# Kernel tuning notes

Hardware: AMD Instinct MI355X
Metric: run time of the kernel (lower is better)

Reference implementation:

```python
import jax, jax.numpy as jnp
import numpy as np

NUM_RELATIONS = 4


def setup_inputs() -> dict:
    key = jax.random.key(0)
    ks = jax.random.split(key, 16)
    N, E, IN, H, OUT = 50000, 1000000, 64, 64, 32
    inp = {
        "x": jax.random.normal(ks[0], (N, IN), dtype=jnp.float32),
        "edge_index": jax.random.randint(ks[1], (2, E), 0, N, dtype=jnp.int32),
        "edge_type": jax.random.randint(ks[2], (E,), 0, NUM_RELATIONS, dtype=jnp.int32),
        "edge_weight": jax.random.uniform(ks[3], (E,), dtype=jnp.float32),
        # RGCN layer 1
        "W1": jax.random.normal(ks[4], (NUM_RELATIONS, IN, H), dtype=jnp.float32) * 0.02,
        "W01": jax.random.normal(ks[5], (IN, H), dtype=jnp.float32) * 0.02,
        # GroupEnhance 1
        "alpha1": jnp.float32(0.5),
        "projW1": jax.random.normal(ks[6], (H, H), dtype=jnp.float32) * 0.02,
        "projb1": jnp.zeros((H,), dtype=jnp.float32),
        # RGCN layer 2
        "W2": jax.random.normal(ks[7], (NUM_RELATIONS, H, H), dtype=jnp.float32) * 0.02,
        "W02": jax.random.normal(ks[8], (H, H), dtype=jnp.float32) * 0.02,
        # GroupEnhance 2
        "alpha2": jnp.float32(0.5),
        "projW2": jax.random.normal(ks[9], (H, H), dtype=jnp.float32) * 0.02,
        "projb2": jnp.zeros((H,), dtype=jnp.float32),
        # output head
        "outW": jax.random.normal(ks[10], (H, OUT), dtype=jnp.float32) * 0.02,
        "outb": jnp.zeros((OUT,), dtype=jnp.float32),
    }
    return inp


def _rgcn(x, src, dst, edge_type, edge_weight, W, W0, deg, num_nodes):
    # per-relation transform: msg_e = x[src_e] @ W[edge_type_e]
    xs = x[src]  # [E, d]
    msg = jnp.zeros((xs.shape[0], W.shape[-1]), dtype=x.dtype)
    for r in range(NUM_RELATIONS):
        msg = msg + jnp.where((edge_type == r)[:, None], xs @ W[r], 0.0)
    msg = msg * edge_weight[:, None]
    agg = jax.ops.segment_sum(msg, dst, num_segments=num_nodes)
    out = x @ W0 + agg
    return out / deg[:, None]


def _group(x, src, dst, edge_weight, alpha, projW, projb, deg, num_nodes):
    msg = x[src] * edge_weight[:, None]
    agg = jax.ops.segment_sum(msg, dst, num_segments=num_nodes) / deg[:, None]
    return x + alpha * (agg @ projW + projb)


def reference(x, edge_index, edge_type, edge_weight, W1, W01, alpha1, projW1,
              projb1, W2, W02, alpha2, projW2, projb2, outW, outb):
    num_nodes = x.shape[0]
    src, dst = edge_index[0], edge_index[1]
    # degree (unweighted in-degree, clamped to 1), shared by all layers
    deg = jax.ops.segment_sum(jnp.ones_like(edge_weight), dst,
                              num_segments=num_nodes)
    deg = jnp.clip(deg, 1.0)
    h = jax.nn.relu(_rgcn(x, src, dst, edge_type, edge_weight, W1, W01, deg, num_nodes))
    h = _group(h, src, dst, edge_weight, alpha1, projW1, projb1, deg, num_nodes)
    h = jax.nn.relu(_rgcn(h, src, dst, edge_type, edge_weight, W2, W02, deg, num_nodes))
    h = _group(h, src, dst, edge_weight, alpha2, projW2, projb2, deg, num_nodes)
    return h @ outW + outb
```

## Files before the change

### kernel.cpp

```cpp
#include <hip/hip_runtime.h>


#define PART_EPB 2048

__global__ __launch_bounds__(256) void bucket_hist(const int* __restrict__ ei,
                                                   int* __restrict__ bcnt,
                                                   int E, int NB) {
    __shared__ int h[1024];
    for (int i = threadIdx.x; i < 1024; i += 256) h[i] = 0;
    __syncthreads();
    int base = blockIdx.x * PART_EPB;
#pragma unroll
    for (int k = 0; k < PART_EPB / 256; ++k) {
        int e = base + k * 256 + threadIdx.x;
        if (e < E) atomicAdd(&h[ei[E + e] >> 8], 1);
    }
    __syncthreads();
    for (int i = threadIdx.x; i < NB; i += 256)
        if (h[i]) atomicAdd(&bcnt[i], h[i]);
}

__global__ __launch_bounds__(1024) void bucket_scan(const int* __restrict__ bcnt,
                                                    int* __restrict__ bofs,
                                                    int* __restrict__ bcur,
                                                    int NB, int E) {
    __shared__ int lds[1024];
    int tid = threadIdx.x;
    int v = (tid < NB) ? bcnt[tid] : 0;
    lds[tid] = v;
    __syncthreads();
    int acc = v;
    for (int off = 1; off < 1024; off <<= 1) {
        int t = (tid >= off) ? lds[tid - off] : 0;
        __syncthreads();
        acc += t;
        lds[tid] = acc;
        __syncthreads();
    }
    int excl = acc - v;
    if (tid < NB) { bofs[tid] = excl; bcur[tid] = excl; }
    if (tid == 0) bofs[NB] = E;
}

__global__ __launch_bounds__(256) void partition(const int* __restrict__ ei,
                                                 const int* __restrict__ et,
                                                 const float* __restrict__ ew,
                                                 int* __restrict__ gcur,
                                                 int2* __restrict__ recA,
                                                 int* __restrict__ recB,
                                                 int E, int NB) {
    __shared__ int hist[1024];
    __shared__ int base[1024];
    const int tid = threadIdx.x;
    const int blockBase = blockIdx.x * PART_EPB;
    for (int i = tid; i < 1024; i += 256) hist[i] = 0;
    __syncthreads();
#pragma unroll
    for (int k = 0; k < PART_EPB / 256; ++k) {
        int e = blockBase + k * 256 + tid;
        if (e < E) atomicAdd(&hist[ei[E + e] >> 8], 1);
    }
    __syncthreads();
    for (int i = tid; i < NB; i += 256) {
        int h = hist[i];
        base[i] = h ? atomicAdd(&gcur[i], h) : 0;
    }
    __syncthreads();
    for (int i = tid; i < 1024; i += 256) hist[i] = 0;
    __syncthreads();
#pragma unroll
    for (int k = 0; k < PART_EPB / 256; ++k) {
        int e = blockBase + k * 256 + tid;
        if (e >= E) continue;
        int dst = ei[E + e];
        int b = dst >> 8;
        int pos = base[b] + atomicAdd(&hist[b], 1);
        recA[pos] = make_int2(ei[e], __float_as_int(ew[e]));
        recB[pos] = dst * 4 + et[e];
    }
}

__global__ __launch_bounds__(256) void bucket_fill(
    const int2* __restrict__ recA, const int* __restrict__ recB,
    const int* __restrict__ bofs, int* __restrict__ rp2, int2* __restrict__ pw,
    int N) {
    __shared__ int cnt[1024];
    __shared__ int cur[1024];
    __shared__ int wsum[4];
    const int b = blockIdx.x;
    const int tid = threadIdx.x;
    const int beg = bofs[b], end = bofs[b + 1];
    const int rebase = b << 10;
    for (int j = 0; j < 4; ++j) cnt[tid * 4 + j] = 0;
    __syncthreads();
    for (int i = beg + tid; i < end; i += 256)
        atomicAdd(&cnt[recB[i] - rebase], 1);
    __syncthreads();
    int v[4];
    int s = 0;
#pragma unroll
    for (int j = 0; j < 4; ++j) { v[j] = cnt[tid * 4 + j]; s += v[j]; }
    int lane = tid & 63, wid = tid >> 6;
    int ws = s;
#pragma unroll
    for (int off = 1; off < 64; off <<= 1) {
        int t = __shfl_up(ws, off);
        if (lane >= off) ws += t;
    }
    if (lane == 63) wsum[wid] = ws;
    __syncthreads();
    int wb = 0;
    for (int w = 0; w < wid; ++w) wb += wsum[w];
    int run = beg + wb + ws - s;
#pragma unroll
    for (int j = 0; j < 4; ++j) {
        int idx = rebase + tid * 4 + j;
        if (idx <= 4 * N) rp2[idx] = run;
        cur[tid * 4 + j] = run;
        run += v[j];
    }
    __syncthreads();
    for (int i = beg + tid; i < end; i += 256) {
        int l = recB[i] - rebase;
        int p = atomicAdd(&cur[l], 1);
        pw[p] = recA[i];
    }
}

__device__ __forceinline__ float4 quad_reduce(float4 a) {
#pragma unroll
    for (int off = 16; off < 64; off <<= 1) {
        a.x += __shfl_xor(a.x, off);
        a.y += __shfl_xor(a.y, off);
        a.z += __shfl_xor(a.z, off);
        a.w += __shfl_xor(a.w, off);
    }
    return a;
}

__device__ __forceinline__ void fma4(float4& a, float w, const float4& x) {
    a.x += w * x.x; a.y += w * x.y; a.z += w * x.z; a.w += w * x.w;
}

__device__ __forceinline__ unsigned short f2bf(float f) {
    unsigned u = __float_as_uint(f);
    unsigned r = u + 0x7fffu + ((u >> 16) & 1u);
    return (unsigned short)(r >> 16);
}

__device__ __forceinline__ float bf2f(unsigned short h) {
    return __uint_as_float(((unsigned)h) << 16);
}

__device__ __forceinline__ float4 bf2f4(ushort4 h) {
    return make_float4(bf2f(h.x), bf2f(h.y), bf2f(h.z), bf2f(h.w));
}

__global__ __launch_bounds__(256) void cast_bf16(const float* __restrict__ in,
                                                 unsigned short* __restrict__ out,
                                                 int n4) {
    int i = blockIdx.x * 256 + threadIdx.x;
    if (i >= n4) return;
    float4 v = reinterpret_cast<const float4*>(in)[i];
    reinterpret_cast<ushort4*>(out)[i] =
        make_ushort4(f2bf(v.x), f2bf(v.y), f2bf(v.z), f2bf(v.w));
}

template <int REL>
__global__ __launch_bounds__(256) void gather_k(
    const unsigned short* __restrict__ Xb, const int* __restrict__ rp2,
    const int2* __restrict__ pw, void* __restrict__ outp, int N) {
    int node = blockIdx.x * 4 + (threadIdx.x >> 6);
    if (node >= N) return;
    int lane = threadIdx.x & 63;
    int q = lane >> 4, m = lane & 15;
    const int4 sv = *reinterpret_cast<const int4*>(rp2 + node * 4);
    const int s0 = sv.x, s1 = sv.y, s2 = sv.z, s3 = sv.w;
    const int s4 = rp2[node * 4 + 4];
    float4 A0 = make_float4(0.f, 0.f, 0.f, 0.f);
    float4 A1 = make_float4(0.f, 0.f, 0.f, 0.f);
    float4 A2 = make_float4(0.f, 0.f, 0.f, 0.f);
    float4 A3 = make_float4(0.f, 0.f, 0.f, 0.f);

    auto accum = [&](int idx, int slot, int2 e, const float4& xv) {
        float w = __int_as_float(e.y);
        if (REL) {
            fma4(A0, (idx < s1) ? w : 0.f, xv);
            fma4(A1, (idx >= s1 && idx < s2) ? w : 0.f, xv);
            fma4(A2, (idx >= s2 && idx < s3) ? w : 0.f, xv);
            fma4(A3, (idx >= s3) ? w : 0.f, xv);
        } else {
            if (slot == 0) fma4(A0, w, xv);
            else if (slot == 1) fma4(A1, w, xv);
            else if (slot == 2) fma4(A2, w, xv);
            else fma4(A3, w, xv);
        }
    };

    int i = s0 + q;
    for (; i + 12 < s4; i += 16) {
        int2 e0 = pw[i];
        int2 e1 = pw[i + 4];
        int2 e2 = pw[i + 8];
        int2 e3 = pw[i + 12];
        ushort4 h0 = *reinterpret_cast<const ushort4*>(Xb + (size_t)e0.x * 64 + m * 4);
        ushort4 h1 = *reinterpret_cast<const ushort4*>(Xb + (size_t)e1.x * 64 + m * 4);
        ushort4 h2 = *reinterpret_cast<const ushort4*>(Xb + (size_t)e2.x * 64 + m * 4);
        ushort4 h3 = *reinterpret_cast<const ushort4*>(Xb + (size_t)e3.x * 64 + m * 4);
        accum(i, 0, e0, bf2f4(h0));
        accum(i + 4, 1, e1, bf2f4(h1));
        accum(i + 8, 2, e2, bf2f4(h2));
        accum(i + 12, 3, e3, bf2f4(h3));
    }
    for (; i + 4 < s4; i += 8) {
        int2 e0 = pw[i];
        int2 e1 = pw[i + 4];
        ushort4 h0 = *reinterpret_cast<const ushort4*>(Xb + (size_t)e0.x * 64 + m * 4);
        ushort4 h1 = *reinterpret_cast<const ushort4*>(Xb + (size_t)e1.x * 64 + m * 4);
        accum(i, 0, e0, bf2f4(h0));
        accum(i + 4, 1, e1, bf2f4(h1));
    }
    if (i < s4) {
        int2 e0 = pw[i];
        ushort4 h0 = *reinterpret_cast<const ushort4*>(Xb + (size_t)e0.x * 64 + m * 4);
        accum(i, 0, e0, bf2f4(h0));
    }

    if (REL) {
        A0 = quad_reduce(A0);
        A1 = quad_reduce(A1);
        A2 = quad_reduce(A2);
        A3 = quad_reduce(A3);
        float4 o = (q == 0) ? A0 : (q == 1) ? A1 : (q == 2) ? A2 : A3;
        ushort4 h = make_ushort4(f2bf(o.x), f2bf(o.y), f2bf(o.z), f2bf(o.w));
        *reinterpret_cast<ushort4*>((unsigned short*)outp +
                                    (size_t)node * 256 + q * 64 + m * 4) = h;
    } else {
        A0.x += A1.x + A2.x + A3.x;
        A0.y += A1.y + A2.y + A3.y;
        A0.z += A1.z + A2.z + A3.z;
        A0.w += A1.w + A2.w + A3.w;
        A0 = quad_reduce(A0);
        if (q == 0)
            *reinterpret_cast<float4*>((float*)outp + (size_t)node * 64 + m * 4) = A0;
    }
}

template <int MODE>
__global__ __launch_bounds__(256) void node_gemm(
    const float* __restrict__ X, const float* __restrict__ AGG,
    const unsigned short* __restrict__ AGGh, const float* __restrict__ B0,
    const float* __restrict__ B1, const float* __restrict__ bias,
    const float* __restrict__ bias2, const float* __restrict__ alphap,
    const int* __restrict__ rp2, float* __restrict__ OUT,
    unsigned short* __restrict__ OUTb, int N) {
    __shared__ float As[64][68];
    __shared__ float Bs[64][64];
    const int tid = threadIdx.x;
    const int tx = tid & 15, ty = tid >> 4;
    const int row0 = blockIdx.x * 64;
    float acc[4][4] = {};

    const int nchunks = (MODE == 0) ? 5 : 1;
    for (int c = 0; c < nchunks; ++c) {
        const float* B;
        if (MODE == 0) B = (c == 0) ? B0 : B1 + (size_t)(c - 1) * 64 * 64;
        else           B = B0;
        if (c) __syncthreads();
#pragma unroll
        for (int q = 0; q < 4; ++q) {
            int f = q * 256 + tid;
            int r = f >> 4;
            int c4 = (f & 15) << 2;
            int vr = row0 + r;
            float4 v = make_float4(0.f, 0.f, 0.f, 0.f);
            if (MODE == 0 && c > 0) {
                if (vr < N) {
                    ushort4 hv = *reinterpret_cast<const ushort4*>(
                        AGGh + (size_t)vr * 256 + (c - 1) * 64 + c4);
                    v = bf2f4(hv);
                }
            } else {
                const float* A = (MODE == 0) ? X : AGG;
                if (vr < N) v = *reinterpret_cast<const float4*>(A + (size_t)vr * 64 + c4);
            }
            *reinterpret_cast<float4*>(&As[r][c4]) = v;
            *reinterpret_cast<float4*>(&Bs[r][c4]) =
                *reinterpret_cast<const float4*>(B + (size_t)r * 64 + c4);
        }
        __syncthreads();
#pragma unroll 8
        for (int k = 0; k < 64; ++k) {
            float4 b = *reinterpret_cast<const float4*>(&Bs[k][tx * 4]);
            float a0 = As[ty * 4 + 0][k];
            float a1 = As[ty * 4 + 1][k];
            float a2 = As[ty * 4 + 2][k];
            float a3 = As[ty * 4 + 3][k];
            acc[0][0] += a0 * b.x; acc[0][1] += a0 * b.y; acc[0][2] += a0 * b.z; acc[0][3] += a0 * b.w;
            acc[1][0] += a1 * b.x; acc[1][1] += a1 * b.y; acc[1][2] += a1 * b.z; acc[1][3] += a1 * b.w;
            acc[2][0] += a2 * b.x; acc[2][1] += a2 * b.y; acc[2][2] += a2 * b.z; acc[2][3] += a2 * b.w;
            acc[3][0] += a3 * b.x; acc[3][1] += a3 * b.y; acc[3][2] += a3 * b.z; acc[3][3] += a3 * b.w;
        }
    }

    const float alpha = (MODE == 1 || MODE == 3) ? alphap[0] : 0.f;

    if (MODE == 3) {
        __syncthreads();
#pragma unroll
        for (int i = 0; i < 4; ++i) {
            int vr = row0 + ty * 4 + i;
            float dg = 1.f;
            if (vr < N) dg = fmaxf((float)(rp2[vr * 4 + 4] - rp2[vr * 4]), 1.f);
#pragma unroll
            for (int j = 0; j < 4; ++j) {
                int col = tx * 4 + j;
                float g = 0.f;
                if (vr < N)
                    g = X[(size_t)vr * 64 + col] + alpha * (acc[i][j] / dg + bias[col]);
                As[ty * 4 + i][col] = g;
            }
        }
#pragma unroll
        for (int t = 0; t < 2; ++t) {
            int idx = tid * 2 + t;
            int r = idx >> 3;
            int c4 = (idx & 7) << 2;
            *reinterpret_cast<float4*>(&Bs[r][c4]) =
                *reinterpret_cast<const float4*>(B1 + (size_t)r * 32 + c4);
        }
        __syncthreads();
        float acc2[4][2] = {};
#pragma unroll 8
        for (int k = 0; k < 64; ++k) {
            float b0 = Bs[k][tx * 2];
            float b1 = Bs[k][tx * 2 + 1];
#pragma unroll
            for (int i = 0; i < 4; ++i) {
                float a = As[ty * 4 + i][k];
                acc2[i][0] += a * b0;
                acc2[i][1] += a * b1;
            }
        }
#pragma unroll
        for (int i = 0; i < 4; ++i) {
            int vr = row0 + ty * 4 + i;
            if (vr >= N) continue;
#pragma unroll
            for (int j = 0; j < 2; ++j) {
                int col = tx * 2 + j;
                OUT[(size_t)vr * 32 + col] = acc2[i][j] + bias2[col];
            }
        }
        return;
    }

#pragma unroll
    for (int i = 0; i < 4; ++i) {
        int vr = row0 + ty * 4 + i;
        if (vr >= N) continue;
        float dg = fmaxf((float)(rp2[vr * 4 + 4] - rp2[vr * 4]), 1.f);
        float4 o;
#pragma unroll
        for (int j = 0; j < 4; ++j) {
            int col = tx * 4 + j;
            float v;
            if (MODE == 0) {
                v = fmaxf(acc[i][j] / dg, 0.f);
            } else {
                v = X[(size_t)vr * 64 + col] + alpha * (acc[i][j] / dg + bias[col]);
            }
            OUT[(size_t)vr * 64 + col] = v;
            (&o.x)[j] = v;
        }
        *reinterpret_cast<ushort4*>(OUTb + (size_t)vr * 64 + tx * 4) =
            make_ushort4(f2bf(o.x), f2bf(o.y), f2bf(o.z), f2bf(o.w));
    }
}

extern "C" void kernel_launch(void* const* d_in, const int* in_sizes, int n_in,
                              void* d_out, int out_size, void* d_ws, size_t ws_size,
                              hipStream_t stream) {
    const float* x      = (const float*)d_in[0];
    const int*   ei     = (const int*)d_in[1];
    const int*   et     = (const int*)d_in[2];
    const float* ew     = (const float*)d_in[3];
    const float* W1     = (const float*)d_in[4];
    const float* W01    = (const float*)d_in[5];
    const float* alpha1 = (const float*)d_in[6];
    const float* projW1 = (const float*)d_in[7];
    const float* projb1 = (const float*)d_in[8];
    const float* W2     = (const float*)d_in[9];
    const float* W02    = (const float*)d_in[10];
    const float* alpha2 = (const float*)d_in[11];
    const float* projW2 = (const float*)d_in[12];
    const float* projb2 = (const float*)d_in[13];
    const float* outW   = (const float*)d_in[14];
    const float* outb   = (const float*)d_in[15];
    const int N = in_sizes[0] / 64;
    const int E = in_sizes[2];
    const int M = 4 * N;
    const int NB = (N + 255) >> 8;

    int*   bcnt = (int*)d_ws;
    int*   bofs = bcnt + 1024;
    int*   bcur = bofs + 1032;
    int*   rp2  = bcur + 1024;
    int2*  pw   = (int2*)(rp2 + ((M + 2) & ~1));
    float* aggRegion = (float*)(pw + E);
    unsigned short* aggH = (unsigned short*)aggRegion;
    float* aggF = aggRegion + (size_t)N * 128;
    unsigned short* xb = (unsigned short*)(aggRegion + (size_t)N * 192);
    unsigned short* hb = (unsigned short*)(aggRegion + (size_t)N * 224);
    int2*  recA = (int2*)aggRegion;
    int*   recB = (int*)(recA + E);
    float* hbuf = aggRegion + (size_t)N * 256;
    float* gbuf = hbuf + (size_t)N * 64;

    const int gatherBlocks = (N + 3) / 4;
    const int gemmBlocks = (N + 63) / 64;
    const int pBlocks = (E + PART_EPB - 1) / PART_EPB;

    hipMemsetAsync(bcnt, 0, 1024 * sizeof(int), stream);
    bucket_hist<<<pBlocks, 256, 0, stream>>>(ei, bcnt, E, NB);
    bucket_scan<<<1, 1024, 0, stream>>>(bcnt, bofs, bcur, NB, E);
    partition<<<pBlocks, 256, 0, stream>>>(ei, et, ew, bcur, recA, recB, E, NB);
    bucket_fill<<<NB, 256, 0, stream>>>(recA, recB, bofs, rp2, pw, N);
    cast_bf16<<<(N * 16 + 255) / 256, 256, 0, stream>>>(x, xb, N * 16);

    gather_k<1><<<gatherBlocks, 256, 0, stream>>>(xb, rp2, pw, aggH, N);
    node_gemm<0><<<gemmBlocks, 256, 0, stream>>>(x, nullptr, aggH, W01, W1, nullptr, nullptr, nullptr, rp2, hbuf, hb, N);
    gather_k<0><<<gatherBlocks, 256, 0, stream>>>(hb, rp2, pw, aggF, N);
    node_gemm<1><<<gemmBlocks, 256, 0, stream>>>(hbuf, aggF, nullptr, projW1, nullptr, projb1, nullptr, alpha1, rp2, gbuf, xb , N);

    gather_k<1><<<gatherBlocks, 256, 0, stream>>>(xb , rp2, pw, aggH, N);
    node_gemm<0><<<gemmBlocks, 256, 0, stream>>>(gbuf, nullptr, aggH, W02, W2, nullptr, nullptr, nullptr, rp2, hbuf, hb, N);
    gather_k<0><<<gatherBlocks, 256, 0, stream>>>(hb, rp2, pw, aggF, N);
    node_gemm<3><<<gemmBlocks, 256, 0, stream>>>(hbuf, aggF, nullptr, projW2, outW, projb2, outb, alpha2, rp2, (float*)d_out, nullptr, N);
}
```

Before: 400.2 us.

## Transpose GEMM A tile, register-prefetch next chunk, read bf16 self input

Rewrites the node_gemm inner loop to keep the A tile transposed in shared memory, so each k step reads four rows with one float4 load instead of four scalar loads. In MODE 0 the next chunk's A and B tiles are prefetched into registers while the current chunk computes, which overlaps global loads with FMAs. The self-loop term now reads the bf16 copy of the node features instead of fp32, halving that read but lowering the precision of the root-weight product. The transposed stores into shared memory are scattered and may cause bank conflicts.

Result: slower. 427.0 us (+6.7%).

```diff
diff --git a/kernel.cpp b/kernel.cpp
--- a/kernel.cpp
+++ b/kernel.cpp
@@ -248,58 +248,96 @@
 
 template <int MODE>
 __global__ __launch_bounds__(256) void node_gemm(
-    const float* __restrict__ X, const float* __restrict__ AGG,
-    const unsigned short* __restrict__ AGGh, const float* __restrict__ B0,
-    const float* __restrict__ B1, const float* __restrict__ bias,
-    const float* __restrict__ bias2, const float* __restrict__ alphap,
-    const int* __restrict__ rp2, float* __restrict__ OUT,
-    unsigned short* __restrict__ OUTb, int N) {
-    __shared__ float As[64][68];
+    const float* __restrict__ Xf, const float* __restrict__ AGGf,
+    const unsigned short* __restrict__ Xb0, const unsigned short* __restrict__ AGGh,
+    const float* __restrict__ B0, const float* __restrict__ B1,
+    const float* __restrict__ bias, const float* __restrict__ bias2,
+    const float* __restrict__ alphap, const int* __restrict__ rp2,
+    float* __restrict__ OUT, unsigned short* __restrict__ OUTb, int N) {
+    __shared__ float AsT[64][68];
     __shared__ float Bs[64][64];
     const int tid = threadIdx.x;
     const int tx = tid & 15, ty = tid >> 4;
     const int row0 = blockIdx.x * 64;
     float acc[4][4] = {};
 
-    const int nchunks = (MODE == 0) ? 5 : 1;
-    for (int c = 0; c < nchunks; ++c) {
-        const float* B;
-        if (MODE == 0) B = (c == 0) ? B0 : B1 + (size_t)(c - 1) * 64 * 64;
-        else           B = B0;
-        if (c) __syncthreads();
+    if (MODE == 0) {
+        ushort4 ph[4];
+        float4 pbv[4];
 #pragma unroll
         for (int q = 0; q < 4; ++q) {
             int f = q * 256 + tid;
-            int r = f >> 4;
-            int c4 = (f & 15) << 2;
+            int r = f >> 4, c4 = (f & 15) << 2;
+            int vr = row0 + r;
+            ph[q] = make_ushort4(0, 0, 0, 0);
+            if (vr < N)
+                ph[q] = *reinterpret_cast<const ushort4*>(Xb0 + (size_t)vr * 64 + c4);
+            pbv[q] = *reinterpret_cast<const float4*>(B0 + (size_t)r * 64 + c4);
+        }
+#pragma unroll
+        for (int c = 0; c < 5; ++c) {
+            __syncthreads();
+#pragma unroll
+            for (int q = 0; q < 4; ++q) {
+                int f = q * 256 + tid;
+                int r = f >> 4, c4 = (f & 15) << 2;
+                float4 v = bf2f4(ph[q]);
+                AsT[c4 + 0][r] = v.x;
+                AsT[c4 + 1][r] = v.y;
+                AsT[c4 + 2][r] = v.z;
+                AsT[c4 + 3][r] = v.w;
+                *reinterpret_cast<float4*>(&Bs[r][c4]) = pbv[q];
+            }
+            if (c < 4) {
+                const unsigned short* An = AGGh + (size_t)c * 64;
+                const float* Bn = B1 + (size_t)c * 4096;
+#pragma unroll
+                for (int q = 0; q < 4; ++q) {
+                    int f = q * 256 + tid;
+                    int r = f >> 4, c4 = (f & 15) << 2;
+                    int vr = row0 + r;
+                    ph[q] = make_ushort4(0, 0, 0, 0);
+                    if (vr < N)
+                        ph[q] = *reinterpret_cast<const ushort4*>(
+                            An + (size_t)vr * 256 + c4);
+                    pbv[q] = *reinterpret_cast<const float4*>(Bn + (size_t)r * 64 + c4);
+                }
+            }
+            __syncthreads();
+#pragma unroll 8
+            for (int k = 0; k < 64; ++k) {
+                float4 a = *reinterpret_cast<const float4*>(&AsT[k][ty * 4]);
+                float4 b = *reinterpret_cast<const float4*>(&Bs[k][tx * 4]);
+                acc[0][0] += a.x * b.x; acc[0][1] += a.x * b.y; acc[0][2] += a.x * b.z; acc[0][3] += a.x * b.w;
+                acc[1][0] += a.y * b.x; acc[1][1] += a.y * b.y; acc[1][2] += a.y * b.z; acc[1][3] += a.y * b.w;
+                acc[2][0] += a.z * b.x; acc[2][1] += a.z * b.y; acc[2][2] += a.z * b.z; acc[2][3] += a.z * b.w;
+                acc[3][0] += a.w * b.x; acc[3][1] += a.w * b.y; acc[3][2] += a.w * b.z; acc[3][3] += a.w * b.w;
+            }
+        }
+    } else {
+#pragma unroll
+        for (int q = 0; q < 4; ++q) {
+            int f = q * 256 + tid;
+            int r = f >> 4, c4 = (f & 15) << 2;
             int vr = row0 + r;
             float4 v = make_float4(0.f, 0.f, 0.f, 0.f);
-            if (MODE == 0 && c > 0) {
-                if (vr < N) {
-                    ushort4 hv = *reinterpret_cast<const ushort4*>(
-                        AGGh + (size_t)vr * 256 + (c - 1) * 64 + c4);
-                    v = bf2f4(hv);
-                }
-            } else {
-                const float* A = (MODE == 0) ? X : AGG;
-                if (vr < N) v = *reinterpret_cast<const float4*>(A + (size_t)vr * 64 + c4);
-            }
-            *reinterpret_cast<float4*>(&As[r][c4]) = v;
+            if (vr < N) v = *reinterpret_cast<const float4*>(AGGf + (size_t)vr * 64 + c4);
+            AsT[c4 + 0][r] = v.x;
+            AsT[c4 + 1][r] = v.y;
+            AsT[c4 + 2][r] = v.z;
+            AsT[c4 + 3][r] = v.w;
             *reinterpret_cast<float4*>(&Bs[r][c4]) =
-                *reinterpret_cast<const float4*>(B + (size_t)r * 64 + c4);
+                *reinterpret_cast<const float4*>(B0 + (size_t)r * 64 + c4);
         }
         __syncthreads();
 #pragma unroll 8
         for (int k = 0; k < 64; ++k) {
+            float4 a = *reinterpret_cast<const float4*>(&AsT[k][ty * 4]);
             float4 b = *reinterpret_cast<const float4*>(&Bs[k][tx * 4]);
-            float a0 = As[ty * 4 + 0][k];
-            float a1 = As[ty * 4 + 1][k];
-            float a2 = As[ty * 4 + 2][k];
-            float a3 = As[ty * 4 + 3][k];
-            acc[0][0] += a0 * b.x; acc[0][1] += a0 * b.y; acc[0][2] += a0 * b.z; acc[0][3] += a0 * b.w;
-            acc[1][0] += a1 * b.x; acc[1][1] += a1 * b.y; acc[1][2] += a1 * b.z; acc[1][3] += a1 * b.w;
-            acc[2][0] += a2 * b.x; acc[2][1] += a2 * b.y; acc[2][2] += a2 * b.z; acc[2][3] += a2 * b.w;
-            acc[3][0] += a3 * b.x; acc[3][1] += a3 * b.y; acc[3][2] += a3 * b.z; acc[3][3] += a3 * b.w;
+            acc[0][0] += a.x * b.x; acc[0][1] += a.x * b.y; acc[0][2] += a.x * b.z; acc[0][3] += a.x * b.w;
+            acc[1][0] += a.y * b.x; acc[1][1] += a.y * b.y; acc[1][2] += a.y * b.z; acc[1][3] += a.y * b.w;
+            acc[2][0] += a.z * b.x; acc[2][1] += a.z * b.y; acc[2][2] += a.z * b.z; acc[2][3] += a.z * b.w;
+            acc[3][0] += a.w * b.x; acc[3][1] += a.w * b.y; acc[3][2] += a.w * b.z; acc[3][3] += a.w * b.w;
         }
     }
 
@@ -317,8 +355,8 @@
                 int col = tx * 4 + j;
                 float g = 0.f;
                 if (vr < N)
-                    g = X[(size_t)vr * 64 + col] + alpha * (acc[i][j] / dg + bias[col]);
-                As[ty * 4 + i][col] = g;
+                    g = Xf[(size_t)vr * 64 + col] + alpha * (acc[i][j] / dg + bias[col]);
+                AsT[col][ty * 4 + i] = g;
             }
         }
 #pragma unroll
@@ -333,14 +371,13 @@
         float acc2[4][2] = {};
 #pragma unroll 8
         for (int k = 0; k < 64; ++k) {
+            float4 a = *reinterpret_cast<const float4*>(&AsT[k][ty * 4]);
             float b0 = Bs[k][tx * 2];
             float b1 = Bs[k][tx * 2 + 1];
-#pragma unroll
-            for (int i = 0; i < 4; ++i) {
-                float a = As[ty * 4 + i][k];
-                acc2[i][0] += a * b0;
-                acc2[i][1] += a * b1;
-            }
+            acc2[0][0] += a.x * b0; acc2[0][1] += a.x * b1;
+            acc2[1][0] += a.y * b0; acc2[1][1] += a.y * b1;
+            acc2[2][0] += a.z * b0; acc2[2][1] += a.z * b1;
+            acc2[3][0] += a.w * b0; acc2[3][1] += a.w * b1;
         }
 #pragma unroll
         for (int i = 0; i < 4; ++i) {
@@ -368,7 +405,7 @@
             if (MODE == 0) {
                 v = fmaxf(acc[i][j] / dg, 0.f);
             } else {
-                v = X[(size_t)vr * 64 + col] + alpha * (acc[i][j] / dg + bias[col]);
+                v = Xf[(size_t)vr * 64 + col] + alpha * (acc[i][j] / dg + bias[col]);
             }
             OUT[(size_t)vr * 64 + col] = v;
             (&o.x)[j] = v;
@@ -429,12 +466,12 @@
     cast_bf16<<<(N * 16 + 255) / 256, 256, 0, stream>>>(x, xb, N * 16);
 
     gather_k<1><<<gatherBlocks, 256, 0, stream>>>(xb, rp2, pw, aggH, N);
-    node_gemm<0><<<gemmBlocks, 256, 0, stream>>>(x, nullptr, aggH, W01, W1, nullptr, nullptr, nullptr, rp2, hbuf, hb, N);
+    node_gemm<0><<<gemmBlocks, 256, 0, stream>>>(nullptr, nullptr, xb, aggH, W01, W1, nullptr, nullptr, nullptr, rp2, hbuf, hb, N);
     gather_k<0><<<gatherBlocks, 256, 0, stream>>>(hb, rp2, pw, aggF, N);
-    node_gemm<1><<<gemmBlocks, 256, 0, stream>>>(hbuf, aggF, nullptr, projW1, nullptr, projb1, nullptr, alpha1, rp2, gbuf, xb , N);
+    node_gemm<1><<<gemmBlocks, 256, 0, stream>>>(hbuf, aggF, nullptr, nullptr, projW1, nullptr, projb1, nullptr, alpha1, rp2, gbuf, xb , N);
 
     gather_k<1><<<gatherBlocks, 256, 0, stream>>>(xb , rp2, pw, aggH, N);
-    node_gemm<0><<<gemmBlocks, 256, 0, stream>>>(gbuf, nullptr, aggH, W02, W2, nullptr, nullptr, nullptr, rp2, hbuf, hb, N);
+    node_gemm<0><<<gemmBlocks, 256, 0, stream>>>(nullptr, nullptr, xb, aggH, W02, W2, nullptr, nullptr, nullptr, rp2, hbuf, hb, N);
     gather_k<0><<<gatherBlocks, 256, 0, stream>>>(hb, rp2, pw, aggF, N);
-    node_gemm<3><<<gemmBlocks, 256, 0, stream>>>(hbuf, aggF, nullptr, projW2, outW, projb2, outb, alpha2, rp2, (float*)d_out, nullptr, N);
-}
+    node_gemm<3><<<gemmBlocks, 256, 0, stream>>>(hbuf, aggF, nullptr, nullptr, projW2, outW, projb2, outb, alpha2, rp2, (float*)d_out, nullptr, N);
+}
```

## Run RGCN node GEMM with bf16 MFMA using pre-packed weights

Applied to the files above, without the earlier changes.

Replaces the fp32 LDS-tiled node_gemm<0> (self plus four relation chunks, K=320) with a new kernel that issues bf16 16x16x32 MFMA instructions straight from global memory. Weights are packed once per layer into an MFMA-friendly bf16 layout, and the self-term input is read from the bf16 copy of the activations. This aims to cut the FMA-bound GEMM cost, but it lowers the precision of the self term to bf16 and uses scalar strided output stores.

Measured after the change: 344.7 us. 1.16x faster.

```diff
diff --git a/kernel.cpp b/kernel.cpp
--- a/kernel.cpp
+++ b/kernel.cpp
@@ -2,6 +2,9 @@
 
 
 #define PART_EPB 2048
+
+using short8 = __attribute__((ext_vector_type(8))) short;
+using f32x4v = __attribute__((ext_vector_type(4))) float;
 
 __global__ __launch_bounds__(256) void bucket_hist(const int* __restrict__ ei,
                                                    int* __restrict__ bcnt,
@@ -164,6 +167,18 @@
     float4 v = reinterpret_cast<const float4*>(in)[i];
     reinterpret_cast<ushort4*>(out)[i] =
         make_ushort4(f2bf(v.x), f2bf(v.y), f2bf(v.z), f2bf(v.w));
+}
+
+__global__ __launch_bounds__(256) void pack_w(const float* __restrict__ W0,
+                                              const float* __restrict__ Wr,
+                                              unsigned short* __restrict__ out) {
+    int i = blockIdx.x * 256 + threadIdx.x;
+    if (i >= 20480) return;
+    int j = i & 7, col = (i >> 3) & 15, kg = (i >> 7) & 3, n4 = (i >> 9) & 3, t = i >> 11;
+    int k = t * 32 + kg * 8 + j;
+    int n = n4 * 16 + col;
+    float v = (k < 64) ? W0[k * 64 + n] : Wr[(size_t)(k - 64) * 64 + n];
+    out[i] = f2bf(v);
 }
 
 template <int REL>
@@ -246,14 +261,65 @@
     }
 }
 
+__global__ __launch_bounds__(256) void rgcn_mfma(
+    const unsigned short* __restrict__ Xb, const unsigned short* __restrict__ AGGh,
+    const unsigned short* __restrict__ Bp, const int* __restrict__ rp2,
+    float* __restrict__ OUT, unsigned short* __restrict__ OUTb, int N) {
+    const int tid = threadIdx.x;
+    const int w = tid >> 6, l = tid & 63;
+    const int lr = l & 15, kg = l >> 4;
+    const int rowA = blockIdx.x * 64 + w * 16 + lr;
+    const bool okA = rowA < N;
+    f32x4v acc0 = {0.f, 0.f, 0.f, 0.f};
+    f32x4v acc1 = acc0, acc2 = acc0, acc3 = acc0;
+    const unsigned short* xrow = Xb + (size_t)rowA * 64 + kg * 8;
+    const unsigned short* arow = AGGh + (size_t)rowA * 256 + kg * 8;
+    const unsigned short* bbase = Bp + (size_t)kg * 128 + lr * 8;
+#pragma unroll
+    for (int t = 0; t < 10; ++t) {
+        short8 a = {0, 0, 0, 0, 0, 0, 0, 0};
+        if (okA) {
+            const unsigned short* pa = (t < 2) ? (xrow + t * 32) : (arow + (t - 2) * 32);
+            a = *reinterpret_cast<const short8*>(pa);
+        }
+        short8 b0 = *reinterpret_cast<const short8*>(bbase + (size_t)t * 2048 + 0 * 512);
+        short8 b1 = *reinterpret_cast<const short8*>(bbase + (size_t)t * 2048 + 1 * 512);
+        short8 b2 = *reinterpret_cast<const short8*>(bbase + (size_t)t * 2048 + 2 * 512);
+        short8 b3 = *reinterpret_cast<const short8*>(bbase + (size_t)t * 2048 + 3 * 512);
+        acc0 = __builtin_amdgcn_mfma_f32_16x16x32_bf16(a, b0, acc0, 0, 0, 0);
+        acc1 = __builtin_amdgcn_mfma_f32_16x16x32_bf16(a, b1, acc1, 0, 0, 0);
+        acc2 = __builtin_amdgcn_mfma_f32_16x16x32_bf16(a, b2, acc2, 0, 0, 0);
+        acc3 = __builtin_amdgcn_mfma_f32_16x16x32_bf16(a, b3, acc3, 0, 0, 0);
+    }
+    const int rbase = blockIdx.x * 64 + w * 16 + kg * 4;
+#pragma unroll
+    for (int j = 0; j < 4; ++j) {
+        int row = rbase + j;
+        if (row >= N) continue;
+        float dg = fmaxf((float)(rp2[row * 4 + 4] - rp2[row * 4]), 1.f);
+        float v0 = fmaxf(acc0[j] / dg, 0.f);
+        float v1 = fmaxf(acc1[j] / dg, 0.f);
+        float v2 = fmaxf(acc2[j] / dg, 0.f);
+        float v3 = fmaxf(acc3[j] / dg, 0.f);
+        size_t rb = (size_t)row * 64 + lr;
+        OUT[rb + 0]  = v0;
+        OUT[rb + 16] = v1;
+        OUT[rb + 32] = v2;
+        OUT[rb + 48] = v3;
+        OUTb[rb + 0]  = f2bf(v0);
+        OUTb[rb + 16] = f2bf(v1);
+        OUTb[rb + 32] = f2bf(v2);
+        OUTb[rb + 48] = f2bf(v3);
+    }
+}
+
 template <int MODE>
 __global__ __launch_bounds__(256) void node_gemm(
     const float* __restrict__ X, const float* __restrict__ AGG,
-    const unsigned short* __restrict__ AGGh, const float* __restrict__ B0,
-    const float* __restrict__ B1, const float* __restrict__ bias,
-    const float* __restrict__ bias2, const float* __restrict__ alphap,
-    const int* __restrict__ rp2, float* __restrict__ OUT,
-    unsigned short* __restrict__ OUTb, int N) {
+    const float* __restrict__ B0, const float* __restrict__ B1,
+    const float* __restrict__ bias, const float* __restrict__ bias2,
+    const float* __restrict__ alphap, const int* __restrict__ rp2,
+    float* __restrict__ OUT, unsigned short* __restrict__ OUTb, int N) {
     __shared__ float As[64][68];
     __shared__ float Bs[64][64];
     const int tid = threadIdx.x;
@@ -261,49 +327,32 @@
     const int row0 = blockIdx.x * 64;
     float acc[4][4] = {};
 
-    const int nchunks = (MODE == 0) ? 5 : 1;
-    for (int c = 0; c < nchunks; ++c) {
-        const float* B;
-        if (MODE == 0) B = (c == 0) ? B0 : B1 + (size_t)(c - 1) * 64 * 64;
-        else           B = B0;
-        if (c) __syncthreads();
-#pragma unroll
-        for (int q = 0; q < 4; ++q) {
-            int f = q * 256 + tid;
-            int r = f >> 4;
-            int c4 = (f & 15) << 2;
-            int vr = row0 + r;
-            float4 v = make_float4(0.f, 0.f, 0.f, 0.f);
-            if (MODE == 0 && c > 0) {
-                if (vr < N) {
-                    ushort4 hv = *reinterpret_cast<const ushort4*>(
-                        AGGh + (size_t)vr * 256 + (c - 1) * 64 + c4);
-                    v = bf2f4(hv);
-                }
-            } else {
-                const float* A = (MODE == 0) ? X : AGG;
-                if (vr < N) v = *reinterpret_cast<const float4*>(A + (size_t)vr * 64 + c4);
-            }
-            *reinterpret_cast<float4*>(&As[r][c4]) = v;
-            *reinterpret_cast<float4*>(&Bs[r][c4]) =
-                *reinterpret_cast<const float4*>(B + (size_t)r * 64 + c4);
-        }
-        __syncthreads();
+#pragma unroll
+    for (int q = 0; q < 4; ++q) {
+        int f = q * 256 + tid;
+        int r = f >> 4, c4 = (f & 15) << 2;
+        int vr = row0 + r;
+        float4 v = make_float4(0.f, 0.f, 0.f, 0.f);
+        if (vr < N) v = *reinterpret_cast<const float4*>(AGG + (size_t)vr * 64 + c4);
+        *reinterpret_cast<float4*>(&As[r][c4]) = v;
+        *reinterpret_cast<float4*>(&Bs[r][c4]) =
+            *reinterpret_cast<const float4*>(B0 + (size_t)r * 64 + c4);
+    }
+    __syncthreads();
 #pragma unroll 8
-        for (int k = 0; k < 64; ++k) {
-            float4 b = *reinterpret_cast<const float4*>(&Bs[k][tx * 4]);
-            float a0 = As[ty * 4 + 0][k];
-            float a1 = As[ty * 4 + 1][k];
-            float a2 = As[ty * 4 + 2][k];
-            float a3 = As[ty * 4 + 3][k];
-            acc[0][0] += a0 * b.x; acc[0][1] += a0 * b.y; acc[0][2] += a0 * b.z; acc[0][3] += a0 * b.w;
-            acc[1][0] += a1 * b.x; acc[1][1] += a1 * b.y; acc[1][2] += a1 * b.z; acc[1][3] += a1 * b.w;
-            acc[2][0] += a2 * b.x; acc[2][1] += a2 * b.y; acc[2][2] += a2 * b.z; acc[2][3] += a2 * b.w;
-            acc[3][0] += a3 * b.x; acc[3][1] += a3 * b.y; acc[3][2] += a3 * b.z; acc[3][3] += a3 * b.w;
-        }
-    }
-
-    const float alpha = (MODE == 1 || MODE == 3) ? alphap[0] : 0.f;
+    for (int k = 0; k < 64; ++k) {
+        float4 b = *reinterpret_cast<const float4*>(&Bs[k][tx * 4]);
+        float a0 = As[ty * 4 + 0][k];
+        float a1 = As[ty * 4 + 1][k];
+        float a2 = As[ty * 4 + 2][k];
+        float a3 = As[ty * 4 + 3][k];
+        acc[0][0] += a0 * b.x; acc[0][1] += a0 * b.y; acc[0][2] += a0 * b.z; acc[0][3] += a0 * b.w;
+        acc[1][0] += a1 * b.x; acc[1][1] += a1 * b.y; acc[1][2] += a1 * b.z; acc[1][3] += a1 * b.w;
+        acc[2][0] += a2 * b.x; acc[2][1] += a2 * b.y; acc[2][2] += a2 * b.z; acc[2][3] += a2 * b.w;
+        acc[3][0] += a3 * b.x; acc[3][1] += a3 * b.y; acc[3][2] += a3 * b.z; acc[3][3] += a3 * b.w;
+    }
+
+    const float alpha = alphap[0];
 
     if (MODE == 3) {
         __syncthreads();
@@ -364,12 +413,7 @@
 #pragma unroll
         for (int j = 0; j < 4; ++j) {
             int col = tx * 4 + j;
-            float v;
-            if (MODE == 0) {
-                v = fmaxf(acc[i][j] / dg, 0.f);
-            } else {
-                v = X[(size_t)vr * 64 + col] + alpha * (acc[i][j] / dg + bias[col]);
-            }
+            float v = X[(size_t)vr * 64 + col] + alpha * (acc[i][j] / dg + bias[col]);
             OUT[(size_t)vr * 64 + col] = v;
             (&o.x)[j] = v;
         }
@@ -407,7 +451,7 @@
     int*   bcur = bofs + 1032;
     int*   rp2  = bcur + 1024;
     int2*  pw   = (int2*)(rp2 + ((M + 2) & ~1));
-    float* aggRegion = (float*)(pw + E);
+    float* aggRegion = (float*)(((uintptr_t)(pw + E) + 15) & ~(uintptr_t)15);
     unsigned short* aggH = (unsigned short*)aggRegion;
     float* aggF = aggRegion + (size_t)N * 128;
     unsigned short* xb = (unsigned short*)(aggRegion + (size_t)N * 192);
@@ -416,6 +460,8 @@
     int*   recB = (int*)(recA + E);
     float* hbuf = aggRegion + (size_t)N * 256;
     float* gbuf = hbuf + (size_t)N * 64;
+    unsigned short* wb1 = (unsigned short*)(gbuf + (size_t)N * 64);
+    unsigned short* wb2 = wb1 + 20480;
 
     const int gatherBlocks = (N + 3) / 4;
     const int gemmBlocks = (N + 63) / 64;
@@ -427,14 +473,16 @@
     partition<<<pBlocks, 256, 0, stream>>>(ei, et, ew, bcur, recA, recB, E, NB);
     bucket_fill<<<NB, 256, 0, stream>>>(recA, recB, bofs, rp2, pw, N);
     cast_bf16<<<(N * 16 + 255) / 256, 256, 0, stream>>>(x, xb, N * 16);
+    pack_w<<<80, 256, 0, stream>>>(W01, W1, wb1);
+    pack_w<<<80, 256, 0, stream>>>(W02, W2, wb2);
 
     gather_k<1><<<gatherBlocks, 256, 0, stream>>>(xb, rp2, pw, aggH, N);
-    node_gemm<0><<<gemmBlocks, 256, 0, stream>>>(x, nullptr, aggH, W01, W1, nullptr, nullptr, nullptr, rp2, hbuf, hb, N);
+    rgcn_mfma<<<gemmBlocks, 256, 0, stream>>>(xb, aggH, wb1, rp2, hbuf, hb, N);
     gather_k<0><<<gatherBlocks, 256, 0, stream>>>(hb, rp2, pw, aggF, N);
-    node_gemm<1><<<gemmBlocks, 256, 0, stream>>>(hbuf, aggF, nullptr, projW1, nullptr, projb1, nullptr, alpha1, rp2, gbuf, xb , N);
+    node_gemm<1><<<gemmBlocks, 256, 0, stream>>>(hbuf, aggF, projW1, nullptr, projb1, nullptr, alpha1, rp2, gbuf, xb , N);
 
     gather_k<1><<<gatherBlocks, 256, 0, stream>>>(xb , rp2, pw, aggH, N);
-    node_gemm<0><<<gemmBlocks, 256, 0, stream>>>(gbuf, nullptr, aggH, W02, W2, nullptr, nullptr, nullptr, rp2, hbuf, hb, N);
+    rgcn_mfma<<<gemmBlocks, 256, 0, stream>>>(xb , aggH, wb2, rp2, hbuf, hb, N);
     gather_k<0><<<gatherBlocks, 256, 0, stream>>>(hb, rp2, pw, aggF, N);
-    node_gemm<3><<<gemmBlocks, 256, 0, stream>>>(hbuf, aggF, nullptr, projW2, outW, projb2, outb, alpha2, rp2, (float*)d_out, nullptr, N);
-}
+    node_gemm<3><<<gemmBlocks, 256, 0, stream>>>(hbuf, aggF, projW2, outW, projb2, outb, alpha2, rp2, (float*)d_out, nullptr, N);
+}
```
